# Performance work log

Measured on AMD Instinct MI355X. Metric: run time of the kernel, lower is better.

## Reference

```python
import jax, jax.numpy as jnp
import numpy as np
from jax import lax


def _sobel_kernels3d(n1=1, n2=2, n3=2):
    Sx = np.asarray([[[-n1, 0, n1], [-n2, 0, n2], [-n1, 0, n1]],
                     [[-n2, 0, n2], [-n3 * n2, 0, n3 * n2], [-n2, 0, n2]],
                     [[-n1, 0, n1], [-n2, 0, n2], [-n1, 0, n1]]])
    Sy = np.asarray([[[-n1, -n2, -n1], [0, 0, 0], [n1, n2, n1]],
                     [[-n2, -n3 * n2, -n2], [0, 0, 0], [n2, n3 * n2, n2]],
                     [[-n1, -n2, -n1], [0, 0, 0], [n1, n2, n1]]])
    Sz = np.asarray([[[-n1, -n2, -n1], [-n2, -n3 * n2, -n2], [-n1, -n2, -n1]],
                     [[0, 0, 0], [0, 0, 0], [0, 0, 0]],
                     [[n1, n2, n1], [n2, n3 * n2, n2], [n1, n2, n1]]])
    Sd11 = np.asarray([[[0, n1, n2], [-n1, 0, n1], [-n2, -n1, 0]],
                       [[0, n2, n2 * n3], [-n2, 0, n2], [-n2 * n3, -n2, 0]],
                       [[0, n1, n2], [-n1, 0, n1], [-n2, -n1, 0]]])
    Sd12 = np.asarray([[[-n2, -n1, 0], [-n1, 0, n1], [0, n1, n2]],
                       [[-n2 * n3, -n2, 0], [-n2, 0, n2], [0, n2, n2 * n3]],
                       [[-n2, -n1, 0], [-n1, 0, n1], [0, n1, n2]]])
    Sd21 = Sd11.T
    Sd22 = Sd12.T
    Sd31 = np.asarray([-S.T for S in Sd11.T])
    Sd32 = np.asarray([S.T for S in Sd12.T])
    S = [Sx, Sy, Sz, Sd11, Sd12, Sd21, Sd22, Sd31, Sd32]
    # (9, 1, 3, 3, 3) OIDHW conv weight bank
    return np.stack(S).astype(np.float32)[:, None]


def _grad_edge3d(img, kernels, a=1):
    # img: (B, C, H, W, D); kernels: (9, 1, 3, 3, 3)
    B, C, H, W, D = img.shape
    p = jnp.pad(img, ((0, 0), (0, 0), (a, a), (a, a), (a, a)), mode='reflect')
    Hp, Wp, Dp = H + 2 * a, W + 2 * a, D + 2 * a
    # Each channel convolved independently with all 9 kernels in one conv call.
    xin = p.reshape(B * C, 1, Hp, Wp, Dp)
    conv = lax.conv_general_dilated(
        xin, kernels, window_strides=(1, 1, 1), padding='SAME',
        dimension_numbers=('NCDHW', 'OIDHW', 'NCDHW'))  # (B*C, 9, Hp, Wp, Dp)
    conv = conv.reshape(B, C, 9, Hp, Wp, Dp)
    # torch: sum_c (conv + 1e-6), squared per-filter, then sum_s (. + 1e-6), sqrt, * 1/C
    per_filter = jnp.sum(conv + 1e-6, axis=1)           # (B, 9, Hp, Wp, Dp)
    mag = jnp.sqrt(jnp.sum(per_filter ** 2, axis=1) + 9 * 1e-6) / C  # (B, Hp, Wp, Dp)
    mag = mag[:, a:-a, a:-a, a:-a]                      # (B, H, W, D)
    mn = mag.min()
    mx = mag.max()
    norm = (mag - mn) / (mx - mn + 1e-6)
    return norm.reshape(B, 1, H, W, D)


def setup_inputs() -> dict:
    key = jax.random.key(0)
    kx, ky = jax.random.split(key)
    B, C, H, W, D = 4, 1, 128, 128, 128
    x = jax.random.normal(kx, (B, C, H, W, D), dtype=jnp.float32)
    y = jax.random.normal(ky, (B, C, H, W, D), dtype=jnp.float32)
    kernels = jnp.asarray(_sobel_kernels3d(1, 2, 2))
    return {"x": x, "y": y, "kernels": kernels}


def reference(x, y, kernels):
    edge_x = _grad_edge3d(x, kernels)
    edge_y = _grad_edge3d(y, kernels)
    # lam_errors = [(1.0, L1Loss())], reduction='sum' -> 1e-6 + 1.0 * mean|ex-ey|
    l1 = jnp.mean(jnp.abs(edge_x - edge_y))
    return 1e-6 + 1.0 * l1
```

## Files before the change

### kernel.cpp

```cpp
#include <hip/hip_runtime.h>
#include <hip/hip_fp16.h>

#define HH 128
#define NB 4
#define NVOX (NB * HH * HH * HH)

#define NBLK1 2048
#define GRID2 512
#define TPB 256

__device__ __align__(16) unsigned int g_bmin[NBLK1];
__device__ __align__(16) unsigned int g_bmax[NBLK1];

union U4H8 { uint4 u; __half2 h[4]; };

__global__ __launch_bounds__(256) void pass1_kernel(
    const float* __restrict__ x, const float* __restrict__ y,
    __half* __restrict__ magx, __half* __restrict__ magy,
    float* __restrict__ out) {
    int bid = blockIdx.x;
    int tid = threadIdx.x;
    if (bid == 0 && tid == 0) out[0] = 0.0f;

    int lane = tid & 63, wid = tid >> 6;
    int wg  = bid & 31;
    int hs  = (bid >> 5) & 7;
    int b   = (bid >> 8) & 3;
    int img = bid >> 10;

    const float* __restrict__ src = img ? y : x;
    __half* __restrict__ dst = img ? magy : magx;

    int w  = wg * 4 + wid;
    int wm = (w == 0) ? 1 : (w - 1);
    int wp = (w == 127) ? 126 : (w + 1);
    int h0 = hs << 4;
    const float2* base2 = (const float2*)(src + ((size_t)b << 21));

    float2 sbD[3], ubD[3], dbS[3], sbS[3], ubS[3], dbU[3], sbU[3];
    float mn = 3.4e38f, mx = 0.0f;
    bool l0 = (lane == 0), l63 = (lane == 63);

    auto cstage = [&](float2 q, float2& S, float2& D, float2& U) {
        float Lxs = __shfl_up(q.y, 1);
        float Rys = __shfl_down(q.x, 1);
        float Lx = l0  ? q.y : Lxs;
        float Ry = l63 ? q.x : Rys;
        float tx = Lx + q.y;
        float ty = q.x + Ry;
        S.x = fmaf(2.0f, q.x, tx);
        S.y = fmaf(2.0f, q.y, ty);
        D.x = q.y - Lx;
        D.y = Ry - q.x;
        U.x = tx + q.x;
        U.y = ty + q.y;
    };

#pragma unroll
    for (int r = 0; r < 18; ++r) {
        int hr = h0 + r - 1;
        hr = (hr < 0) ? 1 : ((hr > 127) ? 126 : hr);
        const float2* rm = base2 + (((hr << 7) + wm) << 6);
        const float2* rc = base2 + (((hr << 7) + w)  << 6);
        const float2* rp = base2 + (((hr << 7) + wp) << 6);
        float2 qm = rm[lane], qc = rc[lane], qp = rp[lane];

        float2 S0, D0, U0, S1, D1, U1, S2, D2, U2;
        cstage(qm, S0, D0, U0);
        cstage(qc, S1, D1, U1);
        cstage(qp, S2, D2, U2);

        int slot = r % 3;
        float2 tD = { D0.x + D2.x, D0.y + D2.y };
        sbD[slot] = { fmaf(2.0f, D1.x, tD.x), fmaf(2.0f, D1.y, tD.y) };
        ubD[slot] = { tD.x + D1.x, tD.y + D1.y };
        float2 tS = { S0.x + S2.x, S0.y + S2.y };
        sbS[slot] = { fmaf(2.0f, S1.x, tS.x), fmaf(2.0f, S1.y, tS.y) };
        ubS[slot] = { tS.x + S1.x, tS.y + S1.y };
        dbS[slot] = { S2.x - S0.x, S2.y - S0.y };
        float2 tU = { U0.x + U2.x, U0.y + U2.y };
        sbU[slot] = { fmaf(2.0f, U1.x, tU.x), fmaf(2.0f, U1.y, tU.y) };
        dbU[slot] = { U2.x - U0.x, U2.y - U0.y };

        if (r >= 2) {
            int s0 = (r - 2) % 3, s1 = (r - 1) % 3, s2 = slot;
            float2 m2;
#pragma unroll
            for (int c = 0; c < 2; ++c) {
                float vsbD0 = c ? sbD[s0].y : sbD[s0].x;
                float vsbD1 = c ? sbD[s1].y : sbD[s1].x;
                float vsbD2 = c ? sbD[s2].y : sbD[s2].x;
                float vubD0 = c ? ubD[s0].y : ubD[s0].x;
                float vubD1 = c ? ubD[s1].y : ubD[s1].x;
                float vubD2 = c ? ubD[s2].y : ubD[s2].x;
                float vdbS0 = c ? dbS[s0].y : dbS[s0].x;
                float vdbS1 = c ? dbS[s1].y : dbS[s1].x;
                float vdbS2 = c ? dbS[s2].y : dbS[s2].x;
                float vsbS0 = c ? sbS[s0].y : sbS[s0].x;
                float vsbS2 = c ? sbS[s2].y : sbS[s2].x;
                float vubS0 = c ? ubS[s0].y : ubS[s0].x;
                float vubS2 = c ? ubS[s2].y : ubS[s2].x;
                float vdbU0 = c ? dbU[s0].y : dbU[s0].x;
                float vdbU1 = c ? dbU[s1].y : dbU[s1].x;
                float vdbU2 = c ? dbU[s2].y : dbU[s2].x;
                float vsbU0 = c ? sbU[s0].y : sbU[s0].x;
                float vsbU2 = c ? sbU[s2].y : sbU[s2].x;

                float tsbD = vsbD0 + vsbD2;
                float Gssd = fmaf(2.0f, vsbD1, tsbD);
                float Gusd = tsbD + vsbD1;
                float tubD = vubD0 + vubD2;
                float Gsud = fmaf(2.0f, vubD1, tubD);
                float tdbS = vdbS0 + vdbS2;
                float Gsds = fmaf(2.0f, vdbS1, tdbS);
                float Guds = tdbS + vdbS1;
                float Gdss = vsbS2 - vsbS0;
                float Gdus = vubS2 - vubS0;
                float tdbU = vdbU0 + vdbU2;
                float Gsdu = fmaf(2.0f, vdbU1, tdbU);
                float Gdsu = vsbU2 - vsbU0;

                float f0 = Gssd;
                float f1 = Gsds;
                float f2 = Gdss;
                float f3 = Gsud - Gsdu;
                float f4 = Gsud + Gsdu;
                float f5 = Gdus - Guds;
                float f6 = Gdus + Guds;
                float f7 = Gusd - Gdsu;
                float f8 = Gusd + Gdsu;

                const float e1 = 1e-6f;
                float s = 9.0f * 1e-6f;
                float u;
                u = f0 + e1; s = fmaf(u, u, s);
                u = f1 + e1; s = fmaf(u, u, s);
                u = f2 + e1; s = fmaf(u, u, s);
                u = f3 + e1; s = fmaf(u, u, s);
                u = f4 + e1; s = fmaf(u, u, s);
                u = f5 + e1; s = fmaf(u, u, s);
                u = f6 + e1; s = fmaf(u, u, s);
                u = f7 + e1; s = fmaf(u, u, s);
                u = f8 + e1; s = fmaf(u, u, s);
                float m = sqrtf(s);
                if (c) m2.y = m; else m2.x = m;
            }

            __half2 hm2 = __float22half2_rn(m2);
            float2 mr = __half22float2(hm2);
            int hout = h0 + r - 2;
            int h2idx = (((b * 128 + hout) * 128 + w) << 6) + lane;
            __builtin_nontemporal_store(*(unsigned int*)&hm2,
                (unsigned int*)((__half2*)dst + h2idx));
            mn = fminf(mn, fminf(mr.x, mr.y));
            mx = fmaxf(mx, fmaxf(mr.x, mr.y));
        }
    }

    unsigned int umn = __float_as_uint(mn);
    unsigned int umx = __float_as_uint(mx);
#pragma unroll
    for (int off = 32; off > 0; off >>= 1) {
        unsigned int a1 = __shfl_down(umn, off, 64);
        unsigned int b1 = __shfl_down(umx, off, 64);
        umn = (a1 < umn) ? a1 : umn;
        umx = (b1 > umx) ? b1 : umx;
    }
    __shared__ unsigned int smn[4], smx[4];
    if (lane == 0) { smn[wid] = umn; smx[wid] = umx; }
    __syncthreads();
    if (tid == 0) {
        unsigned int m0 = smn[0] < smn[1] ? smn[0] : smn[1];
        unsigned int m1 = smn[2] < smn[3] ? smn[2] : smn[3];
        unsigned int x0 = smx[0] > smx[1] ? smx[0] : smx[1];
        unsigned int x1 = smx[2] > smx[3] ? smx[2] : smx[3];
        g_bmin[bid] = (m0 < m1 ? m0 : m1);
        g_bmax[bid] = (x0 > x1 ? x0 : x1);
    }
}

__global__ __launch_bounds__(TPB) void pass2_kernel(
    const uint4* __restrict__ magx8, const uint4* __restrict__ magy8,
    float* __restrict__ out) {
    int tid = threadIdx.x, bid = blockIdx.x;
    int lane = tid & 63, wid = tid >> 6;
    __shared__ unsigned int sred[4][4];
    __shared__ float smm[4];
    __shared__ float sv[4];

    const uint4* bmin4 = (const uint4*)g_bmin;
    const uint4* bmax4 = (const uint4*)g_bmax;
    uint4 a = bmin4[tid];
    uint4 b = bmax4[tid];
    uint4 c = bmin4[tid + 256];
    uint4 d = bmax4[tid + 256];
    unsigned int a01 = (a.x < a.y) ? a.x : a.y, a23 = (a.z < a.w) ? a.z : a.w;
    unsigned int b01 = (b.x > b.y) ? b.x : b.y, b23 = (b.z > b.w) ? b.z : b.w;
    unsigned int c01 = (c.x < c.y) ? c.x : c.y, c23 = (c.z < c.w) ? c.z : c.w;
    unsigned int d01 = (d.x > d.y) ? d.x : d.y, d23 = (d.z > d.w) ? d.z : d.w;
    unsigned int v0 = (a01 < a23) ? a01 : a23;
    unsigned int v1 = (b01 > b23) ? b01 : b23;
    unsigned int v2 = (c01 < c23) ? c01 : c23;
    unsigned int v3 = (d01 > d23) ? d01 : d23;
#pragma unroll
    for (int off = 32; off > 0; off >>= 1) {
        unsigned int t0 = __shfl_down(v0, off, 64);
        unsigned int t1 = __shfl_down(v1, off, 64);
        unsigned int t2 = __shfl_down(v2, off, 64);
        unsigned int t3 = __shfl_down(v3, off, 64);
        v0 = (t0 < v0) ? t0 : v0;
        v1 = (t1 > v1) ? t1 : v1;
        v2 = (t2 < v2) ? t2 : v2;
        v3 = (t3 > v3) ? t3 : v3;
    }
    if (lane == 0) { sred[wid][0] = v0; sred[wid][1] = v1; sred[wid][2] = v2; sred[wid][3] = v3; }
    __syncthreads();
    if (tid == 0) {
        unsigned int r0 = sred[0][0], r1 = sred[0][1], r2 = sred[0][2], r3 = sred[0][3];
#pragma unroll
        for (int w = 1; w < 4; ++w) {
            r0 = (sred[w][0] < r0) ? sred[w][0] : r0;
            r1 = (sred[w][1] > r1) ? sred[w][1] : r1;
            r2 = (sred[w][2] < r2) ? sred[w][2] : r2;
            r3 = (sred[w][3] > r3) ? sred[w][3] : r3;
        }
        smm[0] = __uint_as_float(r0);
        smm[1] = __uint_as_float(r1);
        smm[2] = __uint_as_float(r2);
        smm[3] = __uint_as_float(r3);
    }
    __syncthreads();

    float mnx = smm[0], mxx = smm[1], mny = smm[2], mxy = smm[3];
    float ix = 1.0f / (mxx - mnx + 1e-6f);
    float iy = 1.0f / (mxy - mny + 1e-6f);
    float cx = -mnx * ix;
    float cy = -mny * iy;

    float s = 0.0f;
#pragma unroll
    for (int k = 0; k < 8; ++k) {
        int i = bid * 2048 + k * TPB + tid;
        U4H8 qa, qb;
        qa.u = magx8[i];
        qb.u = magy8[i];
#pragma unroll
        for (int j = 0; j < 4; ++j) {
            float2 va = __half22float2(qa.h[j]);
            float2 vb = __half22float2(qb.h[j]);
            s += fabsf(fmaf(va.x, ix, cx) - fmaf(vb.x, iy, cy));
            s += fabsf(fmaf(va.y, ix, cx) - fmaf(vb.y, iy, cy));
        }
    }
#pragma unroll
    for (int off = 32; off > 0; off >>= 1) s += __shfl_down(s, off, 64);
    if (lane == 0) sv[wid] = s;
    __syncthreads();
    if (tid == 0) {
        float partial = ((sv[0] + sv[1]) + (sv[2] + sv[3])) * (1.0f / (float)NVOX);
        if (bid == 0) partial += 1e-6f;
        atomicAdd(out, partial);
    }
}

extern "C" void kernel_launch(void* const* d_in, const int* in_sizes, int n_in,
                              void* d_out, int out_size, void* d_ws, size_t ws_size,
                              hipStream_t stream) {
    const float* x = (const float*)d_in[0];
    const float* y = (const float*)d_in[1];
    float* out = (float*)d_out;

    __half* magx = (__half*)d_ws;
    __half* magy = magx + NVOX;

    pass1_kernel<<<NBLK1, 256, 0, stream>>>(x, y, magx, magy, out);
    pass2_kernel<<<GRID2, TPB, 0, stream>>>((const uint4*)magx, (const uint4*)magy, out);
}
```

Baseline: 143.3 us.

## Compute two adjacent W columns per wavefront to share neighbor column loads

Each wavefront now produces outputs for two adjacent W columns, loading four input rows per H step instead of three for one column. The middle columns' horizontal-stage results are reused across both outputs, and the pass1 grid halves to 1024 blocks with the partial min/max reduction in pass2 adjusted to match. This cuts redundant global loads and cstage work per output, at the cost of more registers per thread and fewer blocks in flight.

```diff
diff --git a/kernel.cpp b/kernel.cpp
--- a/kernel.cpp
+++ b/kernel.cpp
@@ -5,7 +5,7 @@
 #define NB 4
 #define NVOX (NB * HH * HH * HH)
 
-#define NBLK1 2048
+#define NBLK1 1024
 #define GRID2 512
 #define TPB 256
 
@@ -23,21 +23,22 @@
     if (bid == 0 && tid == 0) out[0] = 0.0f;
 
     int lane = tid & 63, wid = tid >> 6;
-    int wg  = bid & 31;
-    int hs  = (bid >> 5) & 7;
-    int b   = (bid >> 8) & 3;
-    int img = bid >> 10;
+    int wg  = bid & 15;
+    int hs  = (bid >> 4) & 7;
+    int b   = (bid >> 7) & 3;
+    int img = bid >> 9;
 
     const float* __restrict__ src = img ? y : x;
     __half* __restrict__ dst = img ? magy : magx;
 
-    int w  = wg * 4 + wid;
-    int wm = (w == 0) ? 1 : (w - 1);
-    int wp = (w == 127) ? 126 : (w + 1);
+    int w0 = wg * 8 + wid * 2;
+    int w1 = w0 + 1;
+    int cw0 = (w0 == 0) ? 1 : (w0 - 1);
+    int cw3 = (w1 == 127) ? 126 : (w1 + 1);
     int h0 = hs << 4;
     const float2* base2 = (const float2*)(src + ((size_t)b << 21));
 
-    float2 sbD[3], ubD[3], dbS[3], sbS[3], ubS[3], dbU[3], sbU[3];
+    float2 sbD[2][3], ubD[2][3], dbS[2][3], sbS[2][3], ubS[2][3], dbU[2][3], sbU[2][3];
     float mn = 3.4e38f, mx = 0.0f;
     bool l0 = (lane == 0), l63 = (lane == 63);
 
@@ -60,100 +61,111 @@
     for (int r = 0; r < 18; ++r) {
         int hr = h0 + r - 1;
         hr = (hr < 0) ? 1 : ((hr > 127) ? 126 : hr);
-        const float2* rm = base2 + (((hr << 7) + wm) << 6);
-        const float2* rc = base2 + (((hr << 7) + w)  << 6);
-        const float2* rp = base2 + (((hr << 7) + wp) << 6);
-        float2 qm = rm[lane], qc = rc[lane], qp = rp[lane];
-
-        float2 S0, D0, U0, S1, D1, U1, S2, D2, U2;
-        cstage(qm, S0, D0, U0);
-        cstage(qc, S1, D1, U1);
-        cstage(qp, S2, D2, U2);
+        int rowb = (hr << 7);
+        float2 q0 = base2[(size_t)((rowb + cw0) << 6) + lane];
+        float2 q1 = base2[(size_t)((rowb + w0)  << 6) + lane];
+        float2 q2 = base2[(size_t)((rowb + w1)  << 6) + lane];
+        float2 q3 = base2[(size_t)((rowb + cw3) << 6) + lane];
+
+        float2 S[4], D[4], U[4];
+        cstage(q0, S[0], D[0], U[0]);
+        cstage(q1, S[1], D[1], U[1]);
+        cstage(q2, S[2], D[2], U[2]);
+        cstage(q3, S[3], D[3], U[3]);
 
         int slot = r % 3;
-        float2 tD = { D0.x + D2.x, D0.y + D2.y };
-        sbD[slot] = { fmaf(2.0f, D1.x, tD.x), fmaf(2.0f, D1.y, tD.y) };
-        ubD[slot] = { tD.x + D1.x, tD.y + D1.y };
-        float2 tS = { S0.x + S2.x, S0.y + S2.y };
-        sbS[slot] = { fmaf(2.0f, S1.x, tS.x), fmaf(2.0f, S1.y, tS.y) };
-        ubS[slot] = { tS.x + S1.x, tS.y + S1.y };
-        dbS[slot] = { S2.x - S0.x, S2.y - S0.y };
-        float2 tU = { U0.x + U2.x, U0.y + U2.y };
-        sbU[slot] = { fmaf(2.0f, U1.x, tU.x), fmaf(2.0f, U1.y, tU.y) };
-        dbU[slot] = { U2.x - U0.x, U2.y - U0.y };
+#pragma unroll
+        for (int o = 0; o < 2; ++o) {
+            float2 D0 = D[o], D1 = D[o + 1], D2 = D[o + 2];
+            float2 S0 = S[o], S1 = S[o + 1], S2 = S[o + 2];
+            float2 U0 = U[o], U1 = U[o + 1], U2 = U[o + 2];
+            float2 tD = { D0.x + D2.x, D0.y + D2.y };
+            sbD[o][slot] = { fmaf(2.0f, D1.x, tD.x), fmaf(2.0f, D1.y, tD.y) };
+            ubD[o][slot] = { tD.x + D1.x, tD.y + D1.y };
+            float2 tS = { S0.x + S2.x, S0.y + S2.y };
+            sbS[o][slot] = { fmaf(2.0f, S1.x, tS.x), fmaf(2.0f, S1.y, tS.y) };
+            ubS[o][slot] = { tS.x + S1.x, tS.y + S1.y };
+            dbS[o][slot] = { S2.x - S0.x, S2.y - S0.y };
+            float2 tU = { U0.x + U2.x, U0.y + U2.y };
+            sbU[o][slot] = { fmaf(2.0f, U1.x, tU.x), fmaf(2.0f, U1.y, tU.y) };
+            dbU[o][slot] = { U2.x - U0.x, U2.y - U0.y };
+        }
 
         if (r >= 2) {
             int s0 = (r - 2) % 3, s1 = (r - 1) % 3, s2 = slot;
-            float2 m2;
-#pragma unroll
-            for (int c = 0; c < 2; ++c) {
-                float vsbD0 = c ? sbD[s0].y : sbD[s0].x;
-                float vsbD1 = c ? sbD[s1].y : sbD[s1].x;
-                float vsbD2 = c ? sbD[s2].y : sbD[s2].x;
-                float vubD0 = c ? ubD[s0].y : ubD[s0].x;
-                float vubD1 = c ? ubD[s1].y : ubD[s1].x;
-                float vubD2 = c ? ubD[s2].y : ubD[s2].x;
-                float vdbS0 = c ? dbS[s0].y : dbS[s0].x;
-                float vdbS1 = c ? dbS[s1].y : dbS[s1].x;
-                float vdbS2 = c ? dbS[s2].y : dbS[s2].x;
-                float vsbS0 = c ? sbS[s0].y : sbS[s0].x;
-                float vsbS2 = c ? sbS[s2].y : sbS[s2].x;
-                float vubS0 = c ? ubS[s0].y : ubS[s0].x;
-                float vubS2 = c ? ubS[s2].y : ubS[s2].x;
-                float vdbU0 = c ? dbU[s0].y : dbU[s0].x;
-                float vdbU1 = c ? dbU[s1].y : dbU[s1].x;
-                float vdbU2 = c ? dbU[s2].y : dbU[s2].x;
-                float vsbU0 = c ? sbU[s0].y : sbU[s0].x;
-                float vsbU2 = c ? sbU[s2].y : sbU[s2].x;
-
-                float tsbD = vsbD0 + vsbD2;
-                float Gssd = fmaf(2.0f, vsbD1, tsbD);
-                float Gusd = tsbD + vsbD1;
-                float tubD = vubD0 + vubD2;
-                float Gsud = fmaf(2.0f, vubD1, tubD);
-                float tdbS = vdbS0 + vdbS2;
-                float Gsds = fmaf(2.0f, vdbS1, tdbS);
-                float Guds = tdbS + vdbS1;
-                float Gdss = vsbS2 - vsbS0;
-                float Gdus = vubS2 - vubS0;
-                float tdbU = vdbU0 + vdbU2;
-                float Gsdu = fmaf(2.0f, vdbU1, tdbU);
-                float Gdsu = vsbU2 - vsbU0;
-
-                float f0 = Gssd;
-                float f1 = Gsds;
-                float f2 = Gdss;
-                float f3 = Gsud - Gsdu;
-                float f4 = Gsud + Gsdu;
-                float f5 = Gdus - Guds;
-                float f6 = Gdus + Guds;
-                float f7 = Gusd - Gdsu;
-                float f8 = Gusd + Gdsu;
-
-                const float e1 = 1e-6f;
-                float s = 9.0f * 1e-6f;
-                float u;
-                u = f0 + e1; s = fmaf(u, u, s);
-                u = f1 + e1; s = fmaf(u, u, s);
-                u = f2 + e1; s = fmaf(u, u, s);
-                u = f3 + e1; s = fmaf(u, u, s);
-                u = f4 + e1; s = fmaf(u, u, s);
-                u = f5 + e1; s = fmaf(u, u, s);
-                u = f6 + e1; s = fmaf(u, u, s);
-                u = f7 + e1; s = fmaf(u, u, s);
-                u = f8 + e1; s = fmaf(u, u, s);
-                float m = sqrtf(s);
-                if (c) m2.y = m; else m2.x = m;
+            int hout = h0 + r - 2;
+#pragma unroll
+            for (int o = 0; o < 2; ++o) {
+                float2 m2;
+#pragma unroll
+                for (int c = 0; c < 2; ++c) {
+                    float vsbD0 = c ? sbD[o][s0].y : sbD[o][s0].x;
+                    float vsbD1 = c ? sbD[o][s1].y : sbD[o][s1].x;
+                    float vsbD2 = c ? sbD[o][s2].y : sbD[o][s2].x;
+                    float vubD0 = c ? ubD[o][s0].y : ubD[o][s0].x;
+                    float vubD1 = c ? ubD[o][s1].y : ubD[o][s1].x;
+                    float vubD2 = c ? ubD[o][s2].y : ubD[o][s2].x;
+                    float vdbS0 = c ? dbS[o][s0].y : dbS[o][s0].x;
+                    float vdbS1 = c ? dbS[o][s1].y : dbS[o][s1].x;
+                    float vdbS2 = c ? dbS[o][s2].y : dbS[o][s2].x;
+                    float vsbS0 = c ? sbS[o][s0].y : sbS[o][s0].x;
+                    float vsbS2 = c ? sbS[o][s2].y : sbS[o][s2].x;
+                    float vubS0 = c ? ubS[o][s0].y : ubS[o][s0].x;
+                    float vubS2 = c ? ubS[o][s2].y : ubS[o][s2].x;
+                    float vdbU0 = c ? dbU[o][s0].y : dbU[o][s0].x;
+                    float vdbU1 = c ? dbU[o][s1].y : dbU[o][s1].x;
+                    float vdbU2 = c ? dbU[o][s2].y : dbU[o][s2].x;
+                    float vsbU0 = c ? sbU[o][s0].y : sbU[o][s0].x;
+                    float vsbU2 = c ? sbU[o][s2].y : sbU[o][s2].x;
+
+                    float tsbD = vsbD0 + vsbD2;
+                    float Gssd = fmaf(2.0f, vsbD1, tsbD);
+                    float Gusd = tsbD + vsbD1;
+                    float tubD = vubD0 + vubD2;
+                    float Gsud = fmaf(2.0f, vubD1, tubD);
+                    float tdbS = vdbS0 + vdbS2;
+                    float Gsds = fmaf(2.0f, vdbS1, tdbS);
+                    float Guds = tdbS + vdbS1;
+                    float Gdss = vsbS2 - vsbS0;
+                    float Gdus = vubS2 - vubS0;
+                    float tdbU = vdbU0 + vdbU2;
+                    float Gsdu = fmaf(2.0f, vdbU1, tdbU);
+                    float Gdsu = vsbU2 - vsbU0;
+
+                    float f0 = Gssd;
+                    float f1 = Gsds;
+                    float f2 = Gdss;
+                    float f3 = Gsud - Gsdu;
+                    float f4 = Gsud + Gsdu;
+                    float f5 = Gdus - Guds;
+                    float f6 = Gdus + Guds;
+                    float f7 = Gusd - Gdsu;
+                    float f8 = Gusd + Gdsu;
+
+                    const float e1 = 1e-6f;
+                    float s = 9.0f * 1e-6f;
+                    float u;
+                    u = f0 + e1; s = fmaf(u, u, s);
+                    u = f1 + e1; s = fmaf(u, u, s);
+                    u = f2 + e1; s = fmaf(u, u, s);
+                    u = f3 + e1; s = fmaf(u, u, s);
+                    u = f4 + e1; s = fmaf(u, u, s);
+                    u = f5 + e1; s = fmaf(u, u, s);
+                    u = f6 + e1; s = fmaf(u, u, s);
+                    u = f7 + e1; s = fmaf(u, u, s);
+                    u = f8 + e1; s = fmaf(u, u, s);
+                    float m = sqrtf(s);
+                    if (c) m2.y = m; else m2.x = m;
+                }
+
+                __half2 hm2 = __float22half2_rn(m2);
+                float2 mr = __half22float2(hm2);
+                int h2idx = (((b * 128 + hout) * 128 + (w0 + o)) << 6) + lane;
+                __builtin_nontemporal_store(*(unsigned int*)&hm2,
+                    (unsigned int*)((__half2*)dst + h2idx));
+                mn = fminf(mn, fminf(mr.x, mr.y));
+                mx = fmaxf(mx, fmaxf(mr.x, mr.y));
             }
-
-            __half2 hm2 = __float22half2_rn(m2);
-            float2 mr = __half22float2(hm2);
-            int hout = h0 + r - 2;
-            int h2idx = (((b * 128 + hout) * 128 + w) << 6) + lane;
-            __builtin_nontemporal_store(*(unsigned int*)&hm2,
-                (unsigned int*)((__half2*)dst + h2idx));
-            mn = fminf(mn, fminf(mr.x, mr.y));
-            mx = fmaxf(mx, fmaxf(mr.x, mr.y));
         }
     }
 
@@ -190,18 +202,21 @@
 
     const uint4* bmin4 = (const uint4*)g_bmin;
     const uint4* bmax4 = (const uint4*)g_bmax;
-    uint4 a = bmin4[tid];
-    uint4 b = bmax4[tid];
-    uint4 c = bmin4[tid + 256];
-    uint4 d = bmax4[tid + 256];
-    unsigned int a01 = (a.x < a.y) ? a.x : a.y, a23 = (a.z < a.w) ? a.z : a.w;
-    unsigned int b01 = (b.x > b.y) ? b.x : b.y, b23 = (b.z > b.w) ? b.z : b.w;
-    unsigned int c01 = (c.x < c.y) ? c.x : c.y, c23 = (c.z < c.w) ? c.z : c.w;
-    unsigned int d01 = (d.x > d.y) ? d.x : d.y, d23 = (d.z > d.w) ? d.z : d.w;
-    unsigned int v0 = (a01 < a23) ? a01 : a23;
-    unsigned int v1 = (b01 > b23) ? b01 : b23;
-    unsigned int v2 = (c01 < c23) ? c01 : c23;
-    unsigned int v3 = (d01 > d23) ? d01 : d23;
+    unsigned int v0 = 0xFFFFFFFFu, v1 = 0u, v2 = 0xFFFFFFFFu, v3 = 0u;
+    if (tid < 128) {
+        uint4 a = bmin4[tid];
+        uint4 b = bmax4[tid];
+        uint4 c = bmin4[tid + 128];
+        uint4 d = bmax4[tid + 128];
+        unsigned int a01 = (a.x < a.y) ? a.x : a.y, a23 = (a.z < a.w) ? a.z : a.w;
+        unsigned int b01 = (b.x > b.y) ? b.x : b.y, b23 = (b.z > b.w) ? b.z : b.w;
+        unsigned int c01 = (c.x < c.y) ? c.x : c.y, c23 = (c.z < c.w) ? c.z : c.w;
+        unsigned int d01 = (d.x > d.y) ? d.x : d.y, d23 = (d.z > d.w) ? d.z : d.w;
+        v0 = (a01 < a23) ? a01 : a23;
+        v1 = (b01 > b23) ? b01 : b23;
+        v2 = (c01 < c23) ? c01 : c23;
+        v3 = (d01 > d23) ? d01 : d23;
+    }
 #pragma unroll
     for (int off = 32; off > 0; off >>= 1) {
         unsigned int t0 = __shfl_down(v0, off, 64);
```

After: 144.8 us. About the same (+1.0%).
